# Kernel tuning notes

Measured on AMD Instinct MI355X. Metric: run time of the kernel, lower is better.

## Reference

```python
import jax, jax.numpy as jnp
import numpy as np

N = 100000   # nodes of ntype 'gene'
E = 800000   # edges per metapath
D = 256      # input_dim == output_dim
H = 4        # attn heads
C = D // H   # out_channels per head
M = 2        # num metapaths (tail relations = M + 1, last = self)


def _lrelu(x):
    return jnp.where(x >= 0, x, 0.2 * x)


def _segment_softmax(logits, seg, num_segments):
    # logits: [E, H], seg: [E] int targets
    mx = jax.ops.segment_max(logits, seg, num_segments=num_segments)
    mx = jnp.where(jnp.isfinite(mx), mx, 0.0)  # empty segments -> 0
    ex = jnp.exp(logits - mx[seg])
    den = jax.ops.segment_sum(ex, seg, num_segments=num_segments)
    return ex / (den[seg] + 1e-16)


def setup_inputs() -> dict:
    key = jax.random.key(0)
    ks = jax.random.split(key, 10)
    s = 1.0 / np.sqrt(D)
    return {
        "x": jax.random.normal(ks[0], (N, D), dtype=jnp.float32),
        "edge_index0": jax.random.randint(ks[1], (2, E), 0, N, dtype=jnp.int32),
        "edge_index1": jax.random.randint(ks[2], (2, E), 0, N, dtype=jnp.int32),
        "W_l": jax.random.normal(ks[3], (D, D), dtype=jnp.float32) * s,
        "b_l": jnp.zeros((D,), dtype=jnp.float32),
        "W_r": jax.random.normal(ks[4], (D, D), dtype=jnp.float32) * s,
        "b_r": jnp.zeros((D,), dtype=jnp.float32),
        "attn": jax.random.normal(ks[5], (M, H, 2 * C), dtype=jnp.float32) * (1.0 / np.sqrt(2 * C)),
        "rel_attn_l": jax.random.normal(ks[6], (H, C), dtype=jnp.float32) * (1.0 / np.sqrt(C)),
        "rel_attn_r": jax.random.normal(ks[7], (H, C), dtype=jnp.float32) * (1.0 / np.sqrt(C)),
    }


def reference(x, edge_index0, edge_index1, W_l, b_l, W_r, b_r, attn, rel_attn_l, rel_attn_r):
    # projections -> [N, H, C]  (eval mode: dropout/batchnorm off)
    l = (x @ W_l.T + b_l).reshape(N, H, C)
    r = (x @ W_r.T + b_r).reshape(N, H, C)

    # attn split: first C for x_i (target, r-proj), last C for x_j (source, l-proj);
    # leaky_relu is elementwise so the concat+dot separates exactly.
    def agg(edge_index, m_idx):
        src, tgt = edge_index[0], edge_index[1]
        a_i = jnp.einsum('ehc,hc->eh', _lrelu(r[tgt]), attn[m_idx, :, :C])
        a_j = jnp.einsum('ehc,hc->eh', _lrelu(l[src]), attn[m_idx, :, C:])
        alpha = _segment_softmax(a_i + a_j, tgt, N)          # [E, H]
        msg = l[src] * alpha[:, :, None]                      # [E, H, C]
        return jax.ops.segment_sum(msg, tgt, num_segments=N)  # [N, H, C]

    out0 = agg(edge_index0, 0)
    out1 = agg(edge_index1, 1)
    emb = jnp.stack([out0, out1, r], axis=1)                  # [N, M+1, H, C]

    # relation-level beta attention (get_beta_weights)
    alpha_l = jnp.einsum('nhc,hc->nh', r, rel_attn_l)         # [N, H]
    alpha_r = jnp.einsum('nrhc,hc->nrh', emb, rel_attn_r)     # [N, M+1, H]
    beta = jax.nn.softmax(_lrelu(alpha_l[:, None, :] + alpha_r), axis=1)

    h = (emb * beta[..., None]).sum(axis=1).reshape(N, D)
    return jax.nn.relu(h)
```

## Files before the change

### kernel.cpp

```cpp
#include <hip/hip_runtime.h>
#include <hip/hip_bf16.h>
#include <math.h>

#define D_ 256
#define H_ 4
#define C_ 64

typedef __attribute__((ext_vector_type(8))) short short8;
typedef __attribute__((ext_vector_type(4))) float f32x4;

__device__ inline float lrelu(float v) { return v >= 0.f ? v : 0.2f * v; }

__device__ inline unsigned short f2b(float f) {
    unsigned u = __float_as_uint(f);
    u = (u + 0x7FFFu + ((u >> 16) & 1u)) >> 16;
    return (unsigned short)u;
}
__device__ inline float b2f(unsigned short u) {
    return __uint_as_float(((unsigned)u) << 16);
}

#define GLDS(src, dst) __builtin_amdgcn_global_load_lds(                      \
    (const __attribute__((address_space(1))) void*)(src),                     \
    (__attribute__((address_space(3))) void*)(dst), 16, 0, 0)

__global__ __launch_bounds__(256) void convert_w(
    const float* __restrict__ Wl, const float* __restrict__ Wr,
    unsigned short* __restrict__ Wb)
{
    int i4 = blockIdx.x * 256 + threadIdx.x;
    float4 v = (i4 < 16384) ? ((const float4*)Wl)[i4]
                            : ((const float4*)Wr)[i4 - 16384];
    ushort4 u;
    u.x = f2b(v.x); u.y = f2b(v.y); u.z = f2b(v.z); u.w = f2b(v.w);
    ((ushort4*)Wb)[i4] = u;
}

__device__ __forceinline__ void stage_a(const float* __restrict__ x, float* dst,
                                        int bm, int k0, int wv, int lane, int Mrows)
{
#pragma unroll
    for (int p = 0; p < 4; p++) {
        int ci = (p * 4 + wv) * 64 + lane;
        int row = ci >> 3, cc = ci & 7;
        int gr = bm + row; if (gr >= Mrows) gr = Mrows - 1;
        const float* src = x + (size_t)gr * 256 + k0 + ((cc ^ (row & 7)) << 2);
        GLDS(src, (char*)dst + (size_t)(p * 4 + wv) * 1024);
    }
}
__device__ __forceinline__ void stage_b(const unsigned short* __restrict__ W,
                                        unsigned short* dst, int bn, int k0,
                                        int wv, int lane)
{
#pragma unroll
    for (int p = 0; p < 2; p++) {
        int ci = (p * 4 + wv) * 64 + lane;
        int col = ci >> 2, cc = ci & 3;
        const unsigned short* src = W + (size_t)(bn + col) * 256 + k0 +
                                    ((cc ^ (col & 3)) << 3);
        GLDS(src, (char*)dst + (size_t)(p * 4 + wv) * 1024);
    }
}

template <bool RB16>
__global__ __launch_bounds__(256) void gemm_fused(
    const float* __restrict__ x, const unsigned short* __restrict__ Wb,
    const float* __restrict__ b_l, const float* __restrict__ b_r,
    const float* __restrict__ attn, const float* __restrict__ rel_l,
    const float* __restrict__ rel_r,
    unsigned short* __restrict__ lout, void* __restrict__ rout,
    float2* __restrict__ ej2, float* __restrict__ al, float* __restrict__ rd,
    int Mrows, int nblk)
{
    int hw = blockIdx.x;
    int orig = hw;
    if ((nblk & 7) == 0) {
        int cpx = nblk >> 3;
        orig = (hw & 7) * cpx + (hw >> 3);
    }
    const int sel = (orig & 3) >> 1;
    const int bn = (orig & 1) * 128;
    const int bm = (orig >> 2) * 128;

    __shared__ float As[2][128 * 32];
    __shared__ unsigned short Bs[2][128 * 32];
    const int tid = threadIdx.x;
    const int lane = tid & 63, wv = tid >> 6;
    const int wr = wv >> 1, wc = wv & 1;
    const unsigned short* W = Wb + (size_t)sel * 65536;

    f32x4 acc[4][4];
#pragma unroll
    for (int m = 0; m < 4; m++)
#pragma unroll
        for (int n = 0; n < 4; n++) acc[m][n] = (f32x4)0.f;

    stage_a(x, As[0], bm, 0, wv, lane, Mrows);
    stage_b(W, Bs[0], bn, 0, wv, lane);
    __syncthreads();

    int cur = 0;
#pragma unroll
    for (int t = 0; t < 8; t++) {
        if (t < 7) {
            stage_a(x, As[cur ^ 1], bm, (t + 1) * 32, wv, lane, Mrows);
            stage_b(W, Bs[cur ^ 1], bn, (t + 1) * 32, wv, lane);
        }
        short8 bfr[4];
#pragma unroll
        for (int n = 0; n < 4; n++) {
            int col = wc * 64 + n * 16 + (lane & 15);
            int sc = (lane >> 4) ^ (col & 3);
            bfr[n] = *(const short8*)&Bs[cur][col * 32 + sc * 8];
        }
        short8 afr[4];
#pragma unroll
        for (int m = 0; m < 4; m++) {
            int row = wr * 64 + m * 16 + (lane & 15);
            int c0 = (lane >> 4) * 2;
            const float* ap = &As[cur][row * 32];
            float4 f0 = *(const float4*)&ap[(c0 ^ (row & 7)) << 2];
            float4 f1 = *(const float4*)&ap[((c0 + 1) ^ (row & 7)) << 2];
            union { short8 v; __hip_bfloat162 b2[4]; } u;
            u.b2[0] = __float22bfloat162_rn(make_float2(f0.x, f0.y));
            u.b2[1] = __float22bfloat162_rn(make_float2(f0.z, f0.w));
            u.b2[2] = __float22bfloat162_rn(make_float2(f1.x, f1.y));
            u.b2[3] = __float22bfloat162_rn(make_float2(f1.z, f1.w));
            afr[m] = u.v;
        }
#pragma unroll
        for (int m = 0; m < 4; m++)
#pragma unroll
            for (int n = 0; n < 4; n++)
                acc[m][n] = __builtin_amdgcn_mfma_f32_16x16x32_bf16(
                    afr[m], bfr[n], acc[m][n], 0, 0, 0);
        __syncthreads();
        cur ^= 1;
    }

    const float* bias = sel ? b_r : b_l;
    const int NH = Mrows * H_;
    const int h = (bn >> 6) + wc;
    float bv[4], w0[4], w1[4], w2[4];
    int gcol[4];
#pragma unroll
    for (int n = 0; n < 4; n++) {
        int c = n * 16 + (lane & 15);
        gcol[n] = bn + wc * 64 + c;
        bv[n] = bias[gcol[n]];
        if (sel == 0) {
            w0[n] = attn[(0 * H_ + h) * 128 + 64 + c];
            w1[n] = attn[(1 * H_ + h) * 128 + 64 + c];
            w2[n] = rel_r[h * C_ + c];
        } else {
            w0[n] = rel_l[h * C_ + c];
            w1[n] = rel_r[h * C_ + c];
        }
    }
#pragma unroll
    for (int m = 0; m < 4; m++) {
#pragma unroll
        for (int q = 0; q < 4; q++) {
            int grow = bm + wr * 64 + m * 16 + (lane >> 4) * 4 + q;
            bool ok = grow < Mrows;
            float p0 = 0.f, p1 = 0.f, p2 = 0.f;
#pragma unroll
            for (int n = 0; n < 4; n++) {
                float v = acc[m][n][q] + bv[n];
                if (ok) {
                    if (sel == 0) {
                        lout[(size_t)grow * 256 + gcol[n]] = f2b(v);
                    } else {
                        if (RB16) ((unsigned short*)rout)[(size_t)grow * 256 + gcol[n]] = f2b(v);
                        else      ((float*)rout)[(size_t)grow * 256 + gcol[n]] = v;
                    }
                }
                if (sel == 0) {
                    float lr = lrelu(v);
                    p0 = fmaf(lr, w0[n], p0);
                    p1 = fmaf(lr, w1[n], p1);
                    p2 = fmaf(v, w2[n], p2);
                } else {
                    p0 = fmaf(v, w0[n], p0);
                    p1 = fmaf(v, w1[n], p1);
                }
            }
#pragma unroll
            for (int off = 1; off < 16; off <<= 1) {
                p0 += __shfl_xor(p0, off);
                p1 += __shfl_xor(p1, off);
                if (sel == 0) p2 += __shfl_xor(p2, off);
            }
            if (ok && (lane & 15) == 0) {
                int nh = grow * H_ + h;
                if (sel == 0) {
                    float e0 = __expf(p0), e1 = __expf(p1);
                    ej2[nh]      = make_float2(e0, e0 * p2);
                    ej2[NH + nh] = make_float2(e1, e1 * p2);
                } else {
                    al[nh] = p0;
                    rd[nh] = p1;
                }
            }
        }
    }
}

__global__ __launch_bounds__(256) void edge_hist(
    const int* __restrict__ ei0, const int* __restrict__ ei1,
    int* __restrict__ hist, int E_, int Nn)
{
    int e = blockIdx.x * 256 + threadIdx.x;
    if (e >= E_) return;
    atomicAdd(&hist[ei0[E_ + e]], 1);
    atomicAdd(&hist[Nn + ei1[E_ + e]], 1);
}

__global__ __launch_bounds__(256) void scan_a(
    const int* __restrict__ hist, int* __restrict__ segoff,
    int* __restrict__ bsum, int Nn)
{
    int m = blockIdx.y;
    int gid = blockIdx.x * 256 + threadIdx.x;
    int lane = threadIdx.x & 63, wid = threadIdx.x >> 6;
    int v = (gid < Nn) ? hist[m * Nn + gid] : 0;
    int incl = v;
#pragma unroll
    for (int off = 1; off < 64; off <<= 1) {
        int u = __shfl_up(incl, off);
        if (lane >= off) incl += u;
    }
    __shared__ int ws[4], wo[4];
    if (lane == 63) ws[wid] = incl;
    __syncthreads();
    if (threadIdx.x == 0) {
        int run = 0;
#pragma unroll
        for (int i = 0; i < 4; i++) { wo[i] = run; run += ws[i]; }
        bsum[m * 512 + blockIdx.x] = run;
    }
    __syncthreads();
    if (gid < Nn) segoff[m * Nn + gid] = incl - v + wo[wid];
}

__global__ __launch_bounds__(512) void scan_b(int* __restrict__ bsum, int nb)
{
    int m = blockIdx.x;
    int* b = bsum + m * 512;
    int tid = threadIdx.x, lane = tid & 63, wid = tid >> 6;
    int v = (tid < nb) ? b[tid] : 0;
    int incl = v;
#pragma unroll
    for (int off = 1; off < 64; off <<= 1) {
        int u = __shfl_up(incl, off);
        if (lane >= off) incl += u;
    }
    __shared__ int ws[8], wo[8];
    if (lane == 63) ws[wid] = incl;
    __syncthreads();
    if (tid == 0) {
        int run = 0;
#pragma unroll
        for (int i = 0; i < 8; i++) { wo[i] = run; run += ws[i]; }
    }
    __syncthreads();
    if (tid < nb) b[tid] = incl - v + wo[wid];
}

__global__ __launch_bounds__(256) void edge_scatter(
    const int* __restrict__ ei0, const int* __restrict__ ei1,
    const int* __restrict__ segoff, const int* __restrict__ bsum,
    int* __restrict__ cursor, int* __restrict__ srcs, int E_, int Nn)
{
    int e = blockIdx.x * 256 + threadIdx.x;
    if (e >= E_) return;
    int t0 = ei0[E_ + e];
    int p0 = segoff[t0] + bsum[t0 >> 8] + atomicAdd(&cursor[t0], 1);
    srcs[p0] = ei0[e];
    int t1 = ei1[E_ + e];
    int p1 = segoff[Nn + t1] + bsum[512 + (t1 >> 8)] + atomicAdd(&cursor[Nn + t1], 1);
    srcs[E_ + p1] = ei1[e];
}

template <bool RB16>
__global__ __launch_bounds__(256) void aggregate(
    const int* __restrict__ hist, const int* __restrict__ segoff,
    const int* __restrict__ bsum,
    const int* __restrict__ srcs, const float2* __restrict__ ej2,
    const float* __restrict__ al, const float* __restrict__ rd,
    const void* __restrict__ rv, const unsigned short* __restrict__ l,
    float* __restrict__ out, int Nn, int E_)
{
    int lane = threadIdx.x & 63;
    int t = blockIdx.x * 4 + (threadIdx.x >> 6);
    if (t >= Nn) return;
    int h = lane >> 4;
    int NH = Nn * H_;
    int nh = t * H_ + h;

    float4 rrow;
    if (RB16) {
        ushort4 ru = ((const ushort4*)rv)[(size_t)t * 64 + lane];
        rrow = make_float4(b2f(ru.x), b2f(ru.y), b2f(ru.z), b2f(ru.w));
    } else {
        rrow = ((const float4*)rv)[(size_t)t * 64 + lane];
    }
    float a = al[nh];
    float rdv = rd[nh];

    float4 accm[2];
    float denm[2], pnm[2];
#pragma unroll
    for (int m = 0; m < 2; m++) {
        const int* sp = srcs + (size_t)m * E_;
        const float2* ep = ej2 + (size_t)m * NH;
        int beg = segoff[m * Nn + t] + bsum[m * 512 + (t >> 8)];
        int deg = hist[m * Nn + t];

        float4 aA = make_float4(0.f, 0.f, 0.f, 0.f);
        float4 aB = make_float4(0.f, 0.f, 0.f, 0.f);
        float dA = 0.f, dB = 0.f, pA = 0.f, pB = 0.f;
        int j = 0;
#pragma unroll 2
        for (; j + 1 < deg; j += 2) {
            int s0 = sp[beg + j];
            int s1 = sp[beg + j + 1];
            float2 v0 = ep[(size_t)s0 * H_ + h];
            float2 v1 = ep[(size_t)s1 * H_ + h];
            ushort4 l0 = *(const ushort4*)&l[(size_t)s0 * D_ + lane * 4];
            ushort4 l1 = *(const ushort4*)&l[(size_t)s1 * D_ + lane * 4];
            dA += v0.x; pA += v0.y;
            dB += v1.x; pB += v1.y;
            aA.x = fmaf(b2f(l0.x), v0.x, aA.x);
            aA.y = fmaf(b2f(l0.y), v0.x, aA.y);
            aA.z = fmaf(b2f(l0.z), v0.x, aA.z);
            aA.w = fmaf(b2f(l0.w), v0.x, aA.w);
            aB.x = fmaf(b2f(l1.x), v1.x, aB.x);
            aB.y = fmaf(b2f(l1.y), v1.x, aB.y);
            aB.z = fmaf(b2f(l1.z), v1.x, aB.z);
            aB.w = fmaf(b2f(l1.w), v1.x, aB.w);
        }
        if (j < deg) {
            int s0 = sp[beg + j];
            float2 v0 = ep[(size_t)s0 * H_ + h];
            ushort4 l0 = *(const ushort4*)&l[(size_t)s0 * D_ + lane * 4];
            dA += v0.x; pA += v0.y;
            aA.x = fmaf(b2f(l0.x), v0.x, aA.x);
            aA.y = fmaf(b2f(l0.y), v0.x, aA.y);
            aA.z = fmaf(b2f(l0.z), v0.x, aA.z);
            aA.w = fmaf(b2f(l0.w), v0.x, aA.w);
        }
        accm[m] = make_float4(aA.x + aB.x, aA.y + aB.y, aA.z + aB.z, aA.w + aB.w);
        denm[m] = dA + dB;
        pnm[m] = pA + pB;
    }

    float b0 = lrelu(a + pnm[0] / (denm[0] + 1e-16f));
    float b1 = lrelu(a + pnm[1] / (denm[1] + 1e-16f));
    float b2 = lrelu(a + rdv);
    float mm = fmaxf(b0, fmaxf(b1, b2));
    float e0 = __expf(b0 - mm), e1 = __expf(b1 - mm), e2 = __expf(b2 - mm);
    float inv = 1.f / (e0 + e1 + e2);
    float wm0 = e0 * inv / (denm[0] + 1e-16f);
    float wm1 = e1 * inv / (denm[1] + 1e-16f);
    float b2v = e2 * inv;

    float4 o;
    o.x = fmaxf(fmaf(wm0, accm[0].x, fmaf(wm1, accm[1].x, b2v * rrow.x)), 0.f);
    o.y = fmaxf(fmaf(wm0, accm[0].y, fmaf(wm1, accm[1].y, b2v * rrow.y)), 0.f);
    o.z = fmaxf(fmaf(wm0, accm[0].z, fmaf(wm1, accm[1].z, b2v * rrow.z)), 0.f);
    o.w = fmaxf(fmaf(wm0, accm[0].w, fmaf(wm1, accm[1].w, b2v * rrow.w)), 0.f);
    *(float4*)&out[(size_t)t * D_ + lane * 4] = o;
}

extern "C" void kernel_launch(void* const* d_in, const int* in_sizes, int n_in,
                              void* d_out, int out_size, void* d_ws, size_t ws_size,
                              hipStream_t stream) {
    const float* x     = (const float*)d_in[0];
    const int*   ei0   = (const int*)d_in[1];
    const int*   ei1   = (const int*)d_in[2];
    const float* W_l   = (const float*)d_in[3];
    const float* b_l   = (const float*)d_in[4];
    const float* W_r   = (const float*)d_in[5];
    const float* b_r   = (const float*)d_in[6];
    const float* attn  = (const float*)d_in[7];
    const float* rel_l = (const float*)d_in[8];
    const float* rel_r = (const float*)d_in[9];
    float* out = (float*)d_out;

    const int Nn = in_sizes[0] / D_;
    const int E_ = in_sizes[1] / 2;
    const size_t ND = (size_t)Nn * D_;
    const int NH = Nn * H_;

    char* base = (char*)d_ws;
    unsigned short* l = (unsigned short*)base;      size_t off = ND * 2;
    float2* ej2  = (float2*)(base + off); off += (size_t)2 * NH * 8;
    float* al    = (float*)(base + off);  off += (size_t)NH * 4;
    float* rd    = (float*)(base + off);  off += (size_t)NH * 4;
    int* hist    = (int*)(base + off);    off += (size_t)2 * Nn * 4;
    int* cursor  = (int*)(base + off);    off += (size_t)2 * Nn * 4;
    int* segoff  = (int*)(base + off);    off += (size_t)2 * Nn * 4;
    int* bsum    = (int*)(base + off);    off += (size_t)1024 * 4;
    int* srcs    = (int*)(base + off);    off += (size_t)2 * E_ * 4;
    unsigned short* Wb = (unsigned short*)(base + off); off += (size_t)2 * 65536 * 2;
    unsigned short* rb = (unsigned short*)(base + off);
    const bool rb16 = (ws_size >= off + ND * 2);
    void* r_any = rb16 ? (void*)rb : (void*)out;

    hipMemsetAsync(hist, 0, (size_t)4 * Nn * 4, stream);

    convert_w<<<128, 256, 0, stream>>>(W_l, W_r, Wb);

    int rowTiles = (Nn + 127) / 128;
    int nblk = 4 * rowTiles;
    if (rb16)
        gemm_fused<true ><<<nblk, 256, 0, stream>>>(
            x, Wb, b_l, b_r, attn, rel_l, rel_r, l, r_any, ej2, al, rd, Nn, nblk);
    else
        gemm_fused<false><<<nblk, 256, 0, stream>>>(
            x, Wb, b_l, b_r, attn, rel_l, rel_r, l, r_any, ej2, al, rd, Nn, nblk);

    int eb = (E_ + 255) / 256;
    int nb = (Nn + 255) / 256;
    edge_hist<<<eb, 256, 0, stream>>>(ei0, ei1, hist, E_, Nn);
    scan_a<<<dim3(nb, 2), 256, 0, stream>>>(hist, segoff, bsum, Nn);
    scan_b<<<2, 512, 0, stream>>>(bsum, nb);
    edge_scatter<<<eb, 256, 0, stream>>>(ei0, ei1, segoff, bsum, cursor, srcs, E_, Nn);

    if (rb16)
        aggregate<true ><<<(Nn + 3) / 4, 256, 0, stream>>>(
            hist, segoff, bsum, srcs, ej2, al, rd, r_any, l, out, Nn, E_);
    else
        aggregate<false><<<(Nn + 3) / 4, 256, 0, stream>>>(
            hist, segoff, bsum, srcs, ej2, al, rd, r_any, l, out, Nn, E_);
}
```

Baseline: 438.2 us.

## Convert A tile to bf16 in registers and fuse edge histogram into GEMM launch

```diff
diff --git a/kernel.cpp b/kernel.cpp
--- a/kernel.cpp
+++ b/kernel.cpp
@@ -36,17 +36,35 @@
     ((ushort4*)Wb)[i4] = u;
 }
 
-__device__ __forceinline__ void stage_a(const float* __restrict__ x, float* dst,
-                                        int bm, int k0, int wv, int lane, int Mrows)
-{
-#pragma unroll
-    for (int p = 0; p < 4; p++) {
-        int ci = (p * 4 + wv) * 64 + lane;
-        int row = ci >> 3, cc = ci & 7;
-        int gr = bm + row; if (gr >= Mrows) gr = Mrows - 1;
-        const float* src = x + (size_t)gr * 256 + k0 + ((cc ^ (row & 7)) << 2);
-        GLDS(src, (char*)dst + (size_t)(p * 4 + wv) * 1024);
-    }
+__device__ __forceinline__ void load_a_regs(const float* __restrict__ x,
+                                            int bm, int k0, int tid, int Mrows,
+                                            float4 f[4])
+{
+    int row = tid >> 1;
+    int gr = bm + row; if (gr >= Mrows) gr = Mrows - 1;
+    const float* src = x + (size_t)gr * 256 + k0 + (tid & 1) * 16;
+    f[0] = ((const float4*)src)[0];
+    f[1] = ((const float4*)src)[1];
+    f[2] = ((const float4*)src)[2];
+    f[3] = ((const float4*)src)[3];
+}
+__device__ __forceinline__ void write_a_lds(unsigned short* As, int tid,
+                                            const float4 f[4])
+{
+    int row = tid >> 1;
+    int cc0 = (tid & 1) * 2;
+    int sw = row & 3;
+    union { short8 v; __hip_bfloat162 b[4]; } u0, u1;
+    u0.b[0] = __float22bfloat162_rn(make_float2(f[0].x, f[0].y));
+    u0.b[1] = __float22bfloat162_rn(make_float2(f[0].z, f[0].w));
+    u0.b[2] = __float22bfloat162_rn(make_float2(f[1].x, f[1].y));
+    u0.b[3] = __float22bfloat162_rn(make_float2(f[1].z, f[1].w));
+    u1.b[0] = __float22bfloat162_rn(make_float2(f[2].x, f[2].y));
+    u1.b[1] = __float22bfloat162_rn(make_float2(f[2].z, f[2].w));
+    u1.b[2] = __float22bfloat162_rn(make_float2(f[3].x, f[3].y));
+    u1.b[3] = __float22bfloat162_rn(make_float2(f[3].z, f[3].w));
+    *(short8*)&As[row * 32 + ((cc0 ^ sw) << 3)]       = u0.v;
+    *(short8*)&As[row * 32 + (((cc0 + 1) ^ sw) << 3)] = u1.v;
 }
 __device__ __forceinline__ void stage_b(const unsigned short* __restrict__ W,
                                         unsigned short* dst, int bn, int k0,
@@ -63,15 +81,28 @@
 }
 
 template <bool RB16>
-__global__ __launch_bounds__(256) void gemm_fused(
+__global__ __launch_bounds__(256) void gemm_hist(
     const float* __restrict__ x, const unsigned short* __restrict__ Wb,
     const float* __restrict__ b_l, const float* __restrict__ b_r,
     const float* __restrict__ attn, const float* __restrict__ rel_l,
     const float* __restrict__ rel_r,
     unsigned short* __restrict__ lout, void* __restrict__ rout,
     float2* __restrict__ ej2, float* __restrict__ al, float* __restrict__ rd,
-    int Mrows, int nblk)
-{
+    const int* __restrict__ ei0, const int* __restrict__ ei1,
+    int* __restrict__ hist,
+    int Mrows, int nblk, int E_)
+{
+    const int tid = threadIdx.x;
+
+    if ((int)blockIdx.x >= nblk) {
+        int e = ((int)blockIdx.x - nblk) * 256 + tid;
+        if (e < E_) {
+            atomicAdd(&hist[ei0[E_ + e]], 1);
+            atomicAdd(&hist[Mrows + ei1[E_ + e]], 1);
+        }
+        return;
+    }
+
     int hw = blockIdx.x;
     int orig = hw;
     if ((nblk & 7) == 0) {
@@ -82,9 +113,8 @@
     const int bn = (orig & 1) * 128;
     const int bm = (orig >> 2) * 128;
 
-    __shared__ float As[2][128 * 32];
+    __shared__ unsigned short As[2][128 * 32];
     __shared__ unsigned short Bs[2][128 * 32];
-    const int tid = threadIdx.x;
     const int lane = tid & 63, wv = tid >> 6;
     const int wr = wv >> 1, wc = wv & 1;
     const unsigned short* W = Wb + (size_t)sel * 65536;
@@ -95,38 +125,31 @@
 #pragma unroll
         for (int n = 0; n < 4; n++) acc[m][n] = (f32x4)0.f;
 
-    stage_a(x, As[0], bm, 0, wv, lane, Mrows);
+    float4 fr[4];
+    load_a_regs(x, bm, 0, tid, Mrows, fr);
     stage_b(W, Bs[0], bn, 0, wv, lane);
+    write_a_lds(As[0], tid, fr);
     __syncthreads();
 
     int cur = 0;
 #pragma unroll
     for (int t = 0; t < 8; t++) {
         if (t < 7) {
-            stage_a(x, As[cur ^ 1], bm, (t + 1) * 32, wv, lane, Mrows);
+            load_a_regs(x, bm, (t + 1) * 32, tid, Mrows, fr);
             stage_b(W, Bs[cur ^ 1], bn, (t + 1) * 32, wv, lane);
         }
-        short8 bfr[4];
+        short8 bfr[4], afr[4];
 #pragma unroll
         for (int n = 0; n < 4; n++) {
             int col = wc * 64 + n * 16 + (lane & 15);
             int sc = (lane >> 4) ^ (col & 3);
             bfr[n] = *(const short8*)&Bs[cur][col * 32 + sc * 8];
         }
-        short8 afr[4];
 #pragma unroll
         for (int m = 0; m < 4; m++) {
             int row = wr * 64 + m * 16 + (lane & 15);
-            int c0 = (lane >> 4) * 2;
-            const float* ap = &As[cur][row * 32];
-            float4 f0 = *(const float4*)&ap[(c0 ^ (row & 7)) << 2];
-            float4 f1 = *(const float4*)&ap[((c0 + 1) ^ (row & 7)) << 2];
-            union { short8 v; __hip_bfloat162 b2[4]; } u;
-            u.b2[0] = __float22bfloat162_rn(make_float2(f0.x, f0.y));
-            u.b2[1] = __float22bfloat162_rn(make_float2(f0.z, f0.w));
-            u.b2[2] = __float22bfloat162_rn(make_float2(f1.x, f1.y));
-            u.b2[3] = __float22bfloat162_rn(make_float2(f1.z, f1.w));
-            afr[m] = u.v;
+            int sa = (lane >> 4) ^ (row & 3);
+            afr[m] = *(const short8*)&As[cur][row * 32 + sa * 8];
         }
 #pragma unroll
         for (int m = 0; m < 4; m++)
@@ -134,6 +157,7 @@
             for (int n = 0; n < 4; n++)
                 acc[m][n] = __builtin_amdgcn_mfma_f32_16x16x32_bf16(
                     afr[m], bfr[n], acc[m][n], 0, 0, 0);
+        if (t < 7) write_a_lds(As[cur ^ 1], tid, fr);
         __syncthreads();
         cur ^= 1;
     }
@@ -204,16 +228,6 @@
             }
         }
     }
-}
-
-__global__ __launch_bounds__(256) void edge_hist(
-    const int* __restrict__ ei0, const int* __restrict__ ei1,
-    int* __restrict__ hist, int E_, int Nn)
-{
-    int e = blockIdx.x * 256 + threadIdx.x;
-    if (e >= E_) return;
-    atomicAdd(&hist[ei0[E_ + e]], 1);
-    atomicAdd(&hist[Nn + ei1[E_ + e]], 1);
 }
 
 __global__ __launch_bounds__(256) void scan_a(
@@ -414,16 +428,17 @@
 
     int rowTiles = (Nn + 127) / 128;
     int nblk = 4 * rowTiles;
+    int eb = (E_ + 255) / 256;
     if (rb16)
-        gemm_fused<true ><<<nblk, 256, 0, stream>>>(
-            x, Wb, b_l, b_r, attn, rel_l, rel_r, l, r_any, ej2, al, rd, Nn, nblk);
+        gemm_hist<true ><<<nblk + eb, 256, 0, stream>>>(
+            x, Wb, b_l, b_r, attn, rel_l, rel_r, l, r_any, ej2, al, rd,
+            ei0, ei1, hist, Nn, nblk, E_);
     else
-        gemm_fused<false><<<nblk, 256, 0, stream>>>(
-            x, Wb, b_l, b_r, attn, rel_l, rel_r, l, r_any, ej2, al, rd, Nn, nblk);
-
-    int eb = (E_ + 255) / 256;
+        gemm_hist<false><<<nblk + eb, 256, 0, stream>>>(
+            x, Wb, b_l, b_r, attn, rel_l, rel_r, l, r_any, ej2, al, rd,
+            ei0, ei1, hist, Nn, nblk, E_);
+
     int nb = (Nn + 255) / 256;
-    edge_hist<<<eb, 256, 0, stream>>>(ei0, ei1, hist, E_, Nn);
     scan_a<<<dim3(nb, 2), 256, 0, stream>>>(hist, segoff, bsum, Nn);
     scan_b<<<2, 512, 0, stream>>>(bsum, nb);
     edge_scatter<<<eb, 256, 0, stream>>>(ei0, ei1, segoff, bsum, cursor, srcs, E_, Nn);
```

Result: faster. 427.6 us (-2.4%).

## Fuse edge histogram into GEMM launch and change B-tile LDS swizzle

Applied to the files above, without the earlier changes.

```diff
diff --git a/kernel.cpp b/kernel.cpp
--- a/kernel.cpp
+++ b/kernel.cpp
@@ -57,21 +57,34 @@
         int ci = (p * 4 + wv) * 64 + lane;
         int col = ci >> 2, cc = ci & 3;
         const unsigned short* src = W + (size_t)(bn + col) * 256 + k0 +
-                                    ((cc ^ (col & 3)) << 3);
+                                    ((cc ^ ((col >> 1) & 3)) << 3);
         GLDS(src, (char*)dst + (size_t)(p * 4 + wv) * 1024);
     }
 }
 
 template <bool RB16>
-__global__ __launch_bounds__(256) void gemm_fused(
+__global__ __launch_bounds__(256) void gemm_hist(
     const float* __restrict__ x, const unsigned short* __restrict__ Wb,
     const float* __restrict__ b_l, const float* __restrict__ b_r,
     const float* __restrict__ attn, const float* __restrict__ rel_l,
     const float* __restrict__ rel_r,
     unsigned short* __restrict__ lout, void* __restrict__ rout,
     float2* __restrict__ ej2, float* __restrict__ al, float* __restrict__ rd,
-    int Mrows, int nblk)
-{
+    const int* __restrict__ ei0, const int* __restrict__ ei1,
+    int* __restrict__ hist,
+    int Mrows, int nblk, int E_)
+{
+    const int tid = threadIdx.x;
+
+    if ((int)blockIdx.x >= nblk) {
+        int e = ((int)blockIdx.x - nblk) * 256 + tid;
+        if (e < E_) {
+            atomicAdd(&hist[ei0[E_ + e]], 1);
+            atomicAdd(&hist[Mrows + ei1[E_ + e]], 1);
+        }
+        return;
+    }
+
     int hw = blockIdx.x;
     int orig = hw;
     if ((nblk & 7) == 0) {
@@ -84,7 +97,6 @@
 
     __shared__ float As[2][128 * 32];
     __shared__ unsigned short Bs[2][128 * 32];
-    const int tid = threadIdx.x;
     const int lane = tid & 63, wv = tid >> 6;
     const int wr = wv >> 1, wc = wv & 1;
     const unsigned short* W = Wb + (size_t)sel * 65536;
@@ -110,7 +122,7 @@
 #pragma unroll
         for (int n = 0; n < 4; n++) {
             int col = wc * 64 + n * 16 + (lane & 15);
-            int sc = (lane >> 4) ^ (col & 3);
+            int sc = (lane >> 4) ^ ((col >> 1) & 3);
             bfr[n] = *(const short8*)&Bs[cur][col * 32 + sc * 8];
         }
         short8 afr[4];
@@ -204,16 +216,6 @@
             }
         }
     }
-}
-
-__global__ __launch_bounds__(256) void edge_hist(
-    const int* __restrict__ ei0, const int* __restrict__ ei1,
-    int* __restrict__ hist, int E_, int Nn)
-{
-    int e = blockIdx.x * 256 + threadIdx.x;
-    if (e >= E_) return;
-    atomicAdd(&hist[ei0[E_ + e]], 1);
-    atomicAdd(&hist[Nn + ei1[E_ + e]], 1);
 }
 
 __global__ __launch_bounds__(256) void scan_a(
@@ -414,16 +416,17 @@
 
     int rowTiles = (Nn + 127) / 128;
     int nblk = 4 * rowTiles;
+    int eb = (E_ + 255) / 256;
     if (rb16)
-        gemm_fused<true ><<<nblk, 256, 0, stream>>>(
-            x, Wb, b_l, b_r, attn, rel_l, rel_r, l, r_any, ej2, al, rd, Nn, nblk);
+        gemm_hist<true ><<<nblk + eb, 256, 0, stream>>>(
+            x, Wb, b_l, b_r, attn, rel_l, rel_r, l, r_any, ej2, al, rd,
+            ei0, ei1, hist, Nn, nblk, E_);
     else
-        gemm_fused<false><<<nblk, 256, 0, stream>>>(
-            x, Wb, b_l, b_r, attn, rel_l, rel_r, l, r_any, ej2, al, rd, Nn, nblk);
-
-    int eb = (E_ + 255) / 256;
+        gemm_hist<false><<<nblk + eb, 256, 0, stream>>>(
+            x, Wb, b_l, b_r, attn, rel_l, rel_r, l, r_any, ej2, al, rd,
+            ei0, ei1, hist, Nn, nblk, E_);
+
     int nb = (Nn + 255) / 256;
-    edge_hist<<<eb, 256, 0, stream>>>(ei0, ei1, hist, E_, Nn);
     scan_a<<<dim3(nb, 2), 256, 0, stream>>>(hist, segoff, bsum, Nn);
     scan_b<<<2, 512, 0, stream>>>(bsum, nb);
     edge_scatter<<<eb, 256, 0, stream>>>(ei0, ei1, segoff, bsum, cursor, srcs, E_, Nn);
```

Measured after the change: 420.5 us. 4.0% less time.
